# Performance work log

Hardware: AMD Instinct MI355X
Metric: run time of the kernel (lower is better)

Reference implementation:

```python
import jax, jax.numpy as jnp
import numpy as np

# RWKV6 layer dims (from init_kwargs + fla defaults)
H, DK, DV, NH = 512, 256, 512, 4          # hidden, key_dim, value_dim, heads
HK, HV = DK // NH, DV // NH               # 64, 128
RLOW, WLOW, ID = 32, 64, 1024             # proj_low_rank, decay_low_rank, ffn intermediate
EPS = 1e-5
B, T = 8, 1024


def layernorm(x, g, b):
    m = x.mean(-1, keepdims=True)
    v = ((x - m) ** 2).mean(-1, keepdims=True)
    return (x - m) * jax.lax.rsqrt(v + EPS) * g + b


def token_shift(x):  # shift sequence right by one, zero-pad first token
    return jnp.pad(x, ((0, 0), (1, 0), (0, 0)))[:, :-1]


def rwkv_forward(x, pre_g, pre_b, attn_g, attn_b, ffn_g, ffn_b,
                 xproj_mu, xproj_w1, xproj_w2, x_bias,
                 r_W, w_W1, w_W2, w_b, k_W, v_W, g_W, bonus,
                 gnorm_g, gnorm_b, o_W, fk_mu, fk_W, fv_W, fr_mu, fr_W):
    x0 = layernorm(x, pre_g, pre_b)                 # pre_norm (layer_idx == 0)
    h = layernorm(x0, attn_g, attn_b)               # attn_norm

    # ---- time-mix (RWKV6Attention) ----
    delta = token_shift(h) - h
    # low-rank data-dependent interpolation factors for r,w,k,v,g
    z = jnp.tanh(((h + delta * xproj_mu) @ xproj_w1.T).reshape(B, T, 5, RLOW))
    z = jnp.einsum('blnr,hnr->blnh', z, xproj_w2.reshape(H, 5, RLOW)) + x_bias
    zr, zw, zk, zv, zg = (z[:, :, i] for i in range(5))
    r = ((h + delta * zr) @ r_W.T).reshape(B, T, NH, HK)
    w = jnp.tanh((h + delta * zw) @ w_W1.T) @ w_W2.T + w_b   # decay LoRA
    lw = (-jnp.exp(w)).reshape(B, T, NH, HK)                 # log per-channel decay (< 0)
    k = ((h + delta * zk) @ k_W.T).reshape(B, T, NH, HK)
    v = ((h + delta * zv) @ v_W.T).reshape(B, T, NH, HV)
    g = (h + delta * zg) @ g_W.T

    # WKV6 selective-decay linear recurrence, state S: [B,NH,HK,HV]
    def step(S, inp):
        r_t, k_t, v_t, lw_t = inp
        kv = k_t[..., :, None] * v_t[..., None, :]
        o_t = jnp.einsum('bhk,bhkv->bhv', r_t, S + bonus[None, :, :, None] * kv)
        return jnp.exp(lw_t)[..., None] * S + kv, o_t

    S0 = jnp.zeros((B, NH, HK, HV), x.dtype)
    tfirst = lambda a: jnp.swapaxes(a, 0, 1)
    _, o = jax.lax.scan(step, S0, (tfirst(r), tfirst(k), tfirst(v), tfirst(lw)))
    o = jnp.swapaxes(o, 0, 1)                        # [B,T,NH,HV]

    # GroupNorm(num_heads) over value channels, then swish gate and output proj
    mu = o.mean(-1, keepdims=True)
    var = ((o - mu) ** 2).mean(-1, keepdims=True)
    o = ((o - mu) * jax.lax.rsqrt(var + EPS)).reshape(B, T, DV) * gnorm_g + gnorm_b
    a = (o * (g * jax.nn.sigmoid(g))) @ o_W.T

    res = x0 + a

    # ---- channel-mix (RWKV6FeedForward) ----
    hf = layernorm(res, ffn_g, ffn_b)
    d2 = token_shift(hf) - hf
    kk = jnp.square(jax.nn.relu((hf + d2 * fk_mu) @ fk_W.T))
    val = kk @ fv_W.T
    rec = jax.nn.sigmoid((hf + d2 * fr_mu) @ fr_W.T)
    return res + rec * val


def setup_inputs():
    key = jax.random.key(0)
    ks = iter(jax.random.split(key, 40))
    n = lambda shape, s=0.02: jax.random.normal(next(ks), shape, jnp.float32) * s
    u = lambda shape: jax.random.uniform(next(ks), shape, dtype=jnp.float32)
    return dict(
        x=jax.random.normal(next(ks), (B, T, H), jnp.float32),
        pre_g=jnp.ones(H), pre_b=jnp.zeros(H),
        attn_g=jnp.ones(H), attn_b=jnp.zeros(H),
        ffn_g=jnp.ones(H), ffn_b=jnp.zeros(H),
        xproj_mu=u((H,)), xproj_w1=n((5 * RLOW, H)), xproj_w2=n((H, 5 * RLOW)),
        x_bias=n((5, H)),
        r_W=n((DK, H)),
        w_W1=n((WLOW, H)), w_W2=n((DK, WLOW)), w_b=n((DK,), 0.5),
        k_W=n((DK, H)), v_W=n((DV, H)), g_W=n((DV, H)),
        bonus=n((NH, HK), 0.5),
        gnorm_g=jnp.ones(DV), gnorm_b=jnp.zeros(DV),
        o_W=n((H, DV)),
        fk_mu=u((H,)), fk_W=n((ID, H)),
        fv_W=n((H, ID)),
        fr_mu=u((H,)), fr_W=n((H, H)),
    )


def reference(x, pre_g, pre_b, attn_g, attn_b, ffn_g, ffn_b,
              xproj_mu, xproj_w1, xproj_w2, x_bias,
              r_W, w_W1, w_W2, w_b, k_W, v_W, g_W, bonus,
              gnorm_g, gnorm_b, o_W, fk_mu, fk_W, fv_W, fr_mu, fr_W):
    return rwkv_forward(x, pre_g, pre_b, attn_g, attn_b, ffn_g, ffn_b,
                        xproj_mu, xproj_w1, xproj_w2, x_bias,
                        r_W, w_W1, w_W2, w_b, k_W, v_W, g_W, bonus,
                        gnorm_g, gnorm_b, o_W, fk_mu, fk_W, fv_W, fr_mu, fr_W)
```

## Files before the change

kernel.cpp:

```cpp
#include <hip/hip_runtime.h>


#define DEVINL __device__ __forceinline__

constexpr int B_  = 8, T_ = 1024;
constexpr int BT_ = B_ * T_;
constexpr float EPS_ = 1e-5f;
constexpr int CH_ = 16;
constexpr int NC_ = T_ / CH_;

typedef __bf16 bf16x8 __attribute__((ext_vector_type(8)));
typedef float  f32x4  __attribute__((ext_vector_type(4)));

DEVINL unsigned short f2bs(float f) {
  union { float f; unsigned int i; } c; c.f = f;
  unsigned int x = c.i;
  return (unsigned short)((x + 0x7fffu + ((x >> 16) & 1u)) >> 16);
}
DEVINL float b2f(unsigned short u) {
  union { unsigned int i; float f; } c; c.i = ((unsigned int)u) << 16; return c.f;
}

DEVINL float block_sum256(float v, float* sb) {
  for (int o = 32; o; o >>= 1) v += __shfl_down(v, o);
  int w = threadIdx.x >> 6;
  __syncthreads();
  if ((threadIdx.x & 63) == 0) sb[w] = v;
  __syncthreads();
  return sb[0] + sb[1] + sb[2] + sb[3];
}

DEVINL void gload16(const unsigned short* gsrc, unsigned short* ldsbase) {
  __builtin_amdgcn_global_load_lds(
      (const __attribute__((address_space(1))) unsigned int*)gsrc,
      (__attribute__((address_space(3))) unsigned int*)ldsbase, 16, 0, 0);
}

struct PackSeg { const float* src; int rows, cols, dst_rows; };
struct PackArgs { PackSeg s[12]; int base[13]; };

__global__ __launch_bounds__(256) void pack_kernel(PackArgs pa, unsigned short* dst)
{
  int i = blockIdx.x * 256 + threadIdx.x;
  if (i >= pa.base[12]) return;
  int k = 0;
  while (i >= pa.base[k + 1]) k++;
  int loc = i - pa.base[k];
  PackSeg s = pa.s[k];
  int r = loc / s.cols, c = loc - r * s.cols;
  float v = (r < s.rows) ? s.src[(size_t)r * s.cols + c] : 0.f;
  dst[i] = f2bs(v);
}

__global__ __launch_bounds__(256) void ln2_kernel(
    const float* __restrict__ x,
    const float* __restrict__ pg, const float* __restrict__ pb,
    const float* __restrict__ ag, const float* __restrict__ ab,
    float* __restrict__ x0, unsigned short* __restrict__ h)
{
  __shared__ float sb[4];
  size_t base = (size_t)blockIdx.x * 512;
  int tid = threadIdx.x;
  float v0 = x[base + tid], v1 = x[base + 256 + tid];
  float m = block_sum256(v0 + v1, sb) * (1.f / 512.f);
  float d0 = v0 - m, d1 = v1 - m;
  float var = block_sum256(d0 * d0 + d1 * d1, sb) * (1.f / 512.f);
  float rs = rsqrtf(var + EPS_);
  float a0 = d0 * rs * pg[tid]       + pb[tid];
  float a1 = d1 * rs * pg[tid + 256] + pb[tid + 256];
  x0[base + tid] = a0; x0[base + 256 + tid] = a1;
  float m2 = block_sum256(a0 + a1, sb) * (1.f / 512.f);
  float e0 = a0 - m2, e1 = a1 - m2;
  float var2 = block_sum256(e0 * e0 + e1 * e1, sb) * (1.f / 512.f);
  float rs2 = rsqrtf(var2 + EPS_);
  h[base + tid]       = f2bs(e0 * rs2 * ag[tid]       + ab[tid]);
  h[base + 256 + tid] = f2bs(e1 * rs2 * ag[tid + 256] + ab[tid + 256]);
}

__global__ __launch_bounds__(256) void ln1_kernel(
    const float* __restrict__ in,
    const float* __restrict__ g, const float* __restrict__ b,
    float* __restrict__ out)
{
  __shared__ float sb[4];
  size_t base = (size_t)blockIdx.x * 512;
  int tid = threadIdx.x;
  float v0 = in[base + tid], v1 = in[base + 256 + tid];
  float m = block_sum256(v0 + v1, sb) * (1.f / 512.f);
  float d0 = v0 - m, d1 = v1 - m;
  float var = block_sum256(d0 * d0 + d1 * d1, sb) * (1.f / 512.f);
  float rs = rsqrtf(var + EPS_);
  out[base + tid]       = d0 * rs * g[tid]       + b[tid];
  out[base + 256 + tid] = d1 * rs * g[tid + 256] + b[tid + 256];
}

__global__ __launch_bounds__(256) void ymix_kernel(
    const unsigned short* __restrict__ h, const float* __restrict__ mu,
    unsigned short* __restrict__ y, unsigned short* __restrict__ dl)
{
  int t = blockIdx.x, tid = threadIdx.x, tt = t & (T_ - 1);
  size_t base = (size_t)t * 512;
  for (int c = tid; c < 512; c += 256) {
    float cur  = b2f(h[base + c]);
    float prev = tt ? b2f(h[base - 512 + c]) : 0.f;
    float d = prev - cur;
    dl[base + c] = f2bs(d);
    y[base + c] = f2bs(cur + d * mu[c]);
  }
}

__global__ __launch_bounds__(256) void ffnmix_kernel(
    const float* __restrict__ hf, const float* __restrict__ fkmu,
    const float* __restrict__ frmu,
    unsigned short* __restrict__ mfk, unsigned short* __restrict__ mfr)
{
  int t = blockIdx.x, tid = threadIdx.x, tt = t & (T_ - 1);
  size_t base = (size_t)t * 512;
  for (int c = tid; c < 512; c += 256) {
    float cur  = hf[base + c];
    float prev = tt ? hf[base - 512 + c] : 0.f;
    float d = prev - cur;
    mfk[base + c] = f2bs(cur + d * fkmu[c]);
    mfr[base + c] = f2bs(cur + d * frmu[c]);
  }
}

enum { EP_NONE_F32 = 0, EP_NONE_BF16 = 1, EP_TANH_BF16 = 2, EP_EXPEXP_F32 = 3,
       EP_RES_F32 = 4, EP_RELU2_BF16 = 5, EP_OUT2_F32 = 6, EP_XMIX_BF16 = 7 };

struct GemmDesc {
  const unsigned short* A; const unsigned short* W; void* C;
  const void* bias; const void* aux1; const void* aux2;
  int N, K, lda, ldw, ldc, epi;
};
template <int NG> struct GD { GemmDesc d[NG]; };

template <int BM, int BN, int NG>
__global__ __launch_bounds__(256) void mgemm(GD<NG> p)
{
  GemmDesc dd = p.d[blockIdx.z];
  int n0 = blockIdx.y * BN;
  if (n0 >= dd.N) return;
  int m0 = blockIdx.x * BM;
  constexpr int MFR = BM / 32, NFR = BN / 32;
  constexpr int AIS = BM / 64, WIS = BN / 64;
  constexpr int NLD = AIS + WIS;
  __shared__ unsigned short LDSbuf[2 * (BM + BN) * 32];
  unsigned short* As = LDSbuf;
  unsigned short* Ws = LDSbuf + 2 * BM * 32;
  int tid = threadIdx.x, lane = tid & 63, wid = tid >> 6;
  int wm = wid >> 1, wn = wid & 1, lrow = lane & 15, lkg = lane >> 4;
  int XL = (lrow & 3) ^ ((lrow >> 2) & 3);

  const unsigned short* aSrc[AIS]; int aOff[AIS];
#pragma unroll
  for (int i = 0; i < AIS; i++) {
    int u = i * 256 + wid * 64 + lane;
    int row = u >> 2;
    int kg = (u & 3) ^ (row & 3) ^ ((row >> 2) & 3);
    aSrc[i] = dd.A + (size_t)(m0 + row) * dd.lda + kg * 8;
    aOff[i] = (i * 256 + wid * 64) * 8;
  }
  const unsigned short* wSrc[WIS]; int wOff[WIS];
#pragma unroll
  for (int i = 0; i < WIS; i++) {
    int u = i * 256 + wid * 64 + lane;
    int row = u >> 2;
    int kg = (u & 3) ^ (row & 3) ^ ((row >> 2) & 3);
    wSrc[i] = dd.W + (size_t)(n0 + row) * dd.ldw + kg * 8;
    wOff[i] = (i * 256 + wid * 64) * 8;
  }

  f32x4 acc[MFR][NFR];
#pragma unroll
  for (int mf = 0; mf < MFR; mf++)
#pragma unroll
    for (int nf = 0; nf < NFR; nf++) acc[mf][nf] = (f32x4){0.f, 0.f, 0.f, 0.f};

#pragma unroll
  for (int i = 0; i < AIS; i++) gload16(aSrc[i], As + aOff[i]);
#pragma unroll
  for (int i = 0; i < WIS; i++) gload16(wSrc[i], Ws + wOff[i]);

  int nt = dd.K >> 5;
  for (int t = 0; t < nt; ++t) {
    int cb = t & 1;
    int pbuf = cb ^ 1;
    if (t + 1 < nt) {
      int kb2 = (t + 1) << 5;
      unsigned short* aD = As + pbuf * (BM * 32);
      unsigned short* wD = Ws + pbuf * (BN * 32);
#pragma unroll
      for (int i = 0; i < AIS; i++) gload16(aSrc[i] + kb2, aD + aOff[i]);
#pragma unroll
      for (int i = 0; i < WIS; i++) gload16(wSrc[i] + kb2, wD + wOff[i]);
      if constexpr (NLD == 4) asm volatile("s_waitcnt vmcnt(4)" ::: "memory");
      else                    asm volatile("s_waitcnt vmcnt(2)" ::: "memory");
    } else {
      asm volatile("s_waitcnt vmcnt(0)" ::: "memory");
    }
    __builtin_amdgcn_sched_barrier(0);
    __builtin_amdgcn_s_barrier();

    const unsigned short* AsB = As + cb * (BM * 32);
    const unsigned short* WsB = Ws + cb * (BN * 32);
    bf16x8 bfrag[NFR];
#pragma unroll
    for (int nf = 0; nf < NFR; nf++) {
      int row = (wn * NFR + nf) * 16 + lrow;
      bfrag[nf] = *(const bf16x8*)&WsB[(row * 4 + (lkg ^ XL)) * 8];
    }
#pragma unroll
    for (int mf = 0; mf < MFR; mf++) {
      int row = (wm * MFR + mf) * 16 + lrow;
      bf16x8 afrag = *(const bf16x8*)&AsB[(row * 4 + (lkg ^ XL)) * 8];
#pragma unroll
      for (int nf = 0; nf < NFR; nf++)
        acc[mf][nf] = __builtin_amdgcn_mfma_f32_16x16x32_bf16(
            bfrag[nf], afrag, acc[mf][nf], 0, 0, 0);
    }
    __builtin_amdgcn_sched_barrier(0);
    __builtin_amdgcn_s_barrier();
  }

  bool bf16out = (dd.epi == EP_NONE_BF16 || dd.epi == EP_TANH_BF16 ||
                  dd.epi == EP_RELU2_BF16 || dd.epi == EP_XMIX_BF16);
  if (!bf16out) {
#pragma unroll
    for (int mf = 0; mf < MFR; mf++) {
#pragma unroll
      for (int nf = 0; nf < NFR; nf++) {
        int m  = m0 + wm * (MFR * 16) + mf * 16 + lrow;
        int nb = n0 + wn * (NFR * 16) + nf * 16 + lkg * 4;
        size_t off = (size_t)m * dd.ldc + nb;
        float c0 = acc[mf][nf][0], c1 = acc[mf][nf][1];
        float c2 = acc[mf][nf][2], c3 = acc[mf][nf][3];
        switch (dd.epi) {
          case EP_NONE_F32: {
            f32x4 v = {c0, c1, c2, c3};
            *(f32x4*)((float*)dd.C + off) = v; break;
          }
          case EP_EXPEXP_F32: {
            const float* bi = (const float*)dd.bias;
            f32x4 v = {expf(-expf(c0 + bi[nb + 0])), expf(-expf(c1 + bi[nb + 1])),
                       expf(-expf(c2 + bi[nb + 2])), expf(-expf(c3 + bi[nb + 3]))};
            *(f32x4*)((float*)dd.C + off) = v; break;
          }
          case EP_RES_F32: {
            f32x4 a = *(const f32x4*)((const float*)dd.aux1 + off);
            f32x4 v = {c0 + a[0], c1 + a[1], c2 + a[2], c3 + a[3]};
            *(f32x4*)((float*)dd.C + off) = v; break;
          }
          case EP_OUT2_F32: {
            f32x4 rs = *(const f32x4*)((const float*)dd.aux1 + off);
            f32x4 fr = *(const f32x4*)((const float*)dd.aux2 + off);
            f32x4 v = {rs[0] + (1.f / (1.f + expf(-fr[0]))) * c0,
                       rs[1] + (1.f / (1.f + expf(-fr[1]))) * c1,
                       rs[2] + (1.f / (1.f + expf(-fr[2]))) * c2,
                       rs[3] + (1.f / (1.f + expf(-fr[3]))) * c3};
            *(f32x4*)((float*)dd.C + off) = v; break;
          }
        }
      }
    }
    return;
  }

  unsigned short* Cs = LDSbuf;
#pragma unroll
  for (int mf = 0; mf < MFR; mf++) {
#pragma unroll
    for (int nf = 0; nf < NFR; nf++) {
      int mloc = wm * (MFR * 16) + mf * 16 + lrow;
      int nbl  = wn * (NFR * 16) + nf * 16 + lkg * 4;
      int m = m0 + mloc, nb = n0 + nbl;
      size_t off = (size_t)m * dd.ldc + nb;
      float c0 = acc[mf][nf][0], c1 = acc[mf][nf][1];
      float c2 = acc[mf][nf][2], c3 = acc[mf][nf][3];
      uint2 u;
      switch (dd.epi) {
        case EP_NONE_BF16:
          u.x = f2bs(c0) | ((unsigned)f2bs(c1) << 16);
          u.y = f2bs(c2) | ((unsigned)f2bs(c3) << 16);
          break;
        case EP_TANH_BF16:
          u.x = f2bs(tanhf(c0)) | ((unsigned)f2bs(tanhf(c1)) << 16);
          u.y = f2bs(tanhf(c2)) | ((unsigned)f2bs(tanhf(c3)) << 16);
          break;
        case EP_RELU2_BF16: {
          c0 = fmaxf(c0, 0.f); c1 = fmaxf(c1, 0.f);
          c2 = fmaxf(c2, 0.f); c3 = fmaxf(c3, 0.f);
          u.x = f2bs(c0 * c0) | ((unsigned)f2bs(c1 * c1) << 16);
          u.y = f2bs(c2 * c2) | ((unsigned)f2bs(c3 * c3) << 16);
          break;
        }
        default: {
          const float* bi = (const float*)dd.bias;
          uint2 hv = *(const uint2*)((const unsigned short*)dd.aux1 + off);
          uint2 dv = *(const uint2*)((const unsigned short*)dd.aux2 + off);
          const unsigned short* hu = (const unsigned short*)&hv;
          const unsigned short* du = (const unsigned short*)&dv;
          float r0 = b2f(hu[0]) + b2f(du[0]) * (c0 + bi[nb + 0]);
          float r1 = b2f(hu[1]) + b2f(du[1]) * (c1 + bi[nb + 1]);
          float r2 = b2f(hu[2]) + b2f(du[2]) * (c2 + bi[nb + 2]);
          float r3 = b2f(hu[3]) + b2f(du[3]) * (c3 + bi[nb + 3]);
          u.x = f2bs(r0) | ((unsigned)f2bs(r1) << 16);
          u.y = f2bs(r2) | ((unsigned)f2bs(r3) << 16);
          break;
        }
      }
      int col4 = (nbl >> 2) ^ ((mloc & 7) << 1);
      *(uint2*)&Cs[mloc * BN + col4 * 4] = u;
    }
  }
  __syncthreads();
  constexpr int JW = BN / 8;
  constexpr int UNITS = BM * JW;
  for (int it = tid; it < UNITS; it += 256) {
    int row = it / JW, j = it - row * JW;
    int e = (row & 7) << 1;
    int4 vv = *(const int4*)&Cs[row * BN + (((2 * j) ^ e) << 2)];
    *(int4*)((unsigned short*)dd.C + (size_t)(m0 + row) * dd.ldc + n0 + j * 8) = vv;
  }
}

__global__ __launch_bounds__(256) void rbk_kernel(
    const unsigned short* __restrict__ r, const unsigned short* __restrict__ k,
    const float* __restrict__ bonus, float* __restrict__ rbk)
{
  int t = blockIdx.x, tid = threadIdx.x;
  int hh = tid >> 6, j = tid & 63;
  size_t g = (size_t)t * 256 + hh * 64 + j;
  float p = b2f(r[g]) * b2f(k[g]) * bonus[hh * 64 + j];
  for (int o = 32; o; o >>= 1) p += __shfl_down(p, o);
  if (j == 0) rbk[(size_t)t * 4 + hh] = p;
}

__global__ __launch_bounds__(128) void wkv_pass1(
    const unsigned short* __restrict__ k, const float* __restrict__ ew,
    const unsigned short* __restrict__ v, unsigned short* __restrict__ Sl,
    float* __restrict__ Dp)
{
  __shared__ float kL[CH_][64], eL[CH_][64];
  int blk = blockIdx.x;
  int c = blk & (NC_ - 1), bh = blk >> 6;
  int b = bh >> 2, hh = bh & 3;
  int tid = threadIdx.x;
  size_t tbase = (size_t)b * T_ + (size_t)c * CH_;
  for (int idx = tid; idx < CH_ * 64; idx += 128) {
    int s = idx >> 6, j = idx & 63;
    size_t g = (tbase + s) * 256 + hh * 64 + j;
    kL[s][j] = b2f(k[g]); eL[s][j] = ew[g];
  }
  __syncthreads();
  float S[64];
#pragma unroll
  for (int j = 0; j < 64; j++) S[j] = 0.f;
  for (int s = 0; s < CH_; s++) {
    float vv = b2f(v[(tbase + s) * 512 + hh * 128 + tid]);
    const float4* e4p = (const float4*)&eL[s][0];
    const float4* k4p = (const float4*)&kL[s][0];
#pragma unroll
    for (int q = 0; q < 16; q++) {
      float4 e4 = e4p[q], k4 = k4p[q];
      S[4 * q + 0] = e4.x * S[4 * q + 0] + k4.x * vv;
      S[4 * q + 1] = e4.y * S[4 * q + 1] + k4.y * vv;
      S[4 * q + 2] = e4.z * S[4 * q + 2] + k4.z * vv;
      S[4 * q + 3] = e4.w * S[4 * q + 3] + k4.w * vv;
    }
  }
  size_t sbase = (size_t)blk * 8192;
#pragma unroll
  for (int j = 0; j < 64; j++) Sl[sbase + j * 128 + tid] = f2bs(S[j]);
  if (tid < 64) {
    float d = 1.f;
    for (int s = 0; s < CH_; s++) d *= eL[s][tid];
    Dp[(size_t)blk * 64 + tid] = d;
  }
}

__global__ __launch_bounds__(256) void wkv_scan(
    const unsigned short* __restrict__ Sl, const float* __restrict__ Dp,
    unsigned short* __restrict__ Ss)
{
  int e = blockIdx.x * 256 + threadIdx.x;
  int bh = e >> 13; int kv = e & 8191; int j = kv >> 7;
  float run = 0.f;
  for (int c = 0; c < NC_; c++) {
    size_t base = (size_t)bh * NC_ + c;
    Ss[base * 8192 + kv] = f2bs(run);
    run = Dp[base * 64 + j] * run + b2f(Sl[base * 8192 + kv]);
  }
}

__global__ __launch_bounds__(128) void wkv_pass3(
    const unsigned short* __restrict__ r, const unsigned short* __restrict__ k,
    const float* __restrict__ ew, const unsigned short* __restrict__ v,
    const float* __restrict__ rbk, const unsigned short* __restrict__ Ss,
    float* __restrict__ o)
{
  __shared__ float rL[CH_][64], kL[CH_][64], eL[CH_][64], rbL[CH_];
  int blk = blockIdx.x;
  int c = blk & (NC_ - 1), bh = blk >> 6;
  int b = bh >> 2, hh = bh & 3;
  int tid = threadIdx.x;
  size_t tbase = (size_t)b * T_ + (size_t)c * CH_;
  for (int idx = tid; idx < CH_ * 64; idx += 128) {
    int s = idx >> 6, j = idx & 63;
    size_t g = (tbase + s) * 256 + hh * 64 + j;
    rL[s][j] = b2f(r[g]); kL[s][j] = b2f(k[g]); eL[s][j] = ew[g];
  }
  if (tid < CH_) rbL[tid] = rbk[(tbase + tid) * 4 + hh];
  __syncthreads();
  float S[64];
  size_t sbase = (size_t)blk * 8192;
#pragma unroll
  for (int j = 0; j < 64; j++) S[j] = b2f(Ss[sbase + j * 128 + tid]);
  for (int s = 0; s < CH_; s++) {
    float vv = b2f(v[(tbase + s) * 512 + hh * 128 + tid]);
    float oa = rbL[s] * vv;
    const float4* r4p = (const float4*)&rL[s][0];
    const float4* e4p = (const float4*)&eL[s][0];
    const float4* k4p = (const float4*)&kL[s][0];
#pragma unroll
    for (int q = 0; q < 16; q++) {
      float4 r4 = r4p[q], e4 = e4p[q], k4 = k4p[q];
      oa += r4.x * S[4 * q + 0] + r4.y * S[4 * q + 1]
          + r4.z * S[4 * q + 2] + r4.w * S[4 * q + 3];
      S[4 * q + 0] = e4.x * S[4 * q + 0] + k4.x * vv;
      S[4 * q + 1] = e4.y * S[4 * q + 1] + k4.y * vv;
      S[4 * q + 2] = e4.z * S[4 * q + 2] + k4.z * vv;
      S[4 * q + 3] = e4.w * S[4 * q + 3] + k4.w * vv;
    }
    o[(tbase + s) * 512 + hh * 128 + tid] = oa;
  }
}

__global__ __launch_bounds__(256) void gn_gate_kernel(
    const float* __restrict__ o, const unsigned short* __restrict__ g,
    const float* __restrict__ gg, const float* __restrict__ gb,
    unsigned short* __restrict__ obf)
{
  __shared__ float ov[512], ps[64], qs[64], mh[4], vh[4];
  int t = blockIdx.x, tid = threadIdx.x;
  size_t base = (size_t)t * 512;
  ov[tid] = o[base + tid]; ov[tid + 256] = o[base + 256 + tid];
  __syncthreads();
  if (tid < 64) {
    int hh = tid >> 4, sg = tid & 15;
    const float* p = &ov[hh * 128 + sg * 8];
    float s = 0.f, q = 0.f;
    for (int i = 0; i < 8; i++) { s += p[i]; q += p[i] * p[i]; }
    ps[tid] = s; qs[tid] = q;
  }
  __syncthreads();
  if (tid < 4) {
    float s = 0.f, q = 0.f;
    for (int i = 0; i < 16; i++) { s += ps[tid * 16 + i]; q += qs[tid * 16 + i]; }
    float m = s * (1.f / 128.f);
    mh[tid] = m; vh[tid] = q * (1.f / 128.f) - m * m;
  }
  __syncthreads();
  for (int c = tid; c < 512; c += 256) {
    int hh = c >> 7;
    float nrm = (ov[c] - mh[hh]) * rsqrtf(vh[hh] + EPS_);
    float gv = b2f(g[base + c]);
    float sw = gv * (1.f / (1.f + expf(-gv)));
    obf[base + c] = f2bs((nrm * gg[c] + gb[c]) * sw);
  }
}

extern "C" void kernel_launch(void* const* d_in, const int* in_sizes, int n_in,
                              void* d_out, int out_size, void* d_ws, size_t ws_size,
                              hipStream_t stream) {
  (void)in_sizes; (void)n_in; (void)out_size; (void)ws_size;
  const float* x        = (const float*)d_in[0];
  const float* pre_g    = (const float*)d_in[1];
  const float* pre_b    = (const float*)d_in[2];
  const float* attn_g   = (const float*)d_in[3];
  const float* attn_b   = (const float*)d_in[4];
  const float* ffn_g    = (const float*)d_in[5];
  const float* ffn_b    = (const float*)d_in[6];
  const float* xproj_mu = (const float*)d_in[7];
  const float* xproj_w1 = (const float*)d_in[8];
  const float* xproj_w2 = (const float*)d_in[9];
  const float* x_bias   = (const float*)d_in[10];
  const float* r_W      = (const float*)d_in[11];
  const float* w_W1     = (const float*)d_in[12];
  const float* w_W2     = (const float*)d_in[13];
  const float* w_b      = (const float*)d_in[14];
  const float* k_W      = (const float*)d_in[15];
  const float* v_W      = (const float*)d_in[16];
  const float* g_W      = (const float*)d_in[17];
  const float* bonus    = (const float*)d_in[18];
  const float* gnorm_g  = (const float*)d_in[19];
  const float* gnorm_b  = (const float*)d_in[20];
  const float* o_W      = (const float*)d_in[21];
  const float* fk_mu    = (const float*)d_in[22];
  const float* fk_W     = (const float*)d_in[23];
  const float* fv_W     = (const float*)d_in[24];
  const float* fr_mu    = (const float*)d_in[25];
  const float* fr_W     = (const float*)d_in[26];

  const size_t BTH = (size_t)BT_ * 512;
  size_t cur = 0;
  auto alloc = [&](size_t bytes) { void* p = (char*)d_ws + cur; cur += (bytes + 255) & ~(size_t)255; return p; };
  float*          x0    = (float*)alloc(BTH * 4);
  unsigned short* hbufb = (unsigned short*)alloc(BTH * 2);
  unsigned short* m5b   = (unsigned short*)alloc(5 * BTH * 2);
  unsigned short* rbuf  = (unsigned short*)alloc((size_t)BT_ * 256 * 4);
  unsigned short* kbuf  = (unsigned short*)alloc((size_t)BT_ * 256 * 4);
  float*          ebuf  = (float*)alloc((size_t)BT_ * 256 * 4);
  unsigned short* vbuf  = (unsigned short*)alloc(BTH * 4);
  unsigned short* gbuf  = (unsigned short*)alloc(BTH * 4);
  unsigned short* wtmpb = (unsigned short*)alloc((size_t)BT_ * 128 * 2);
  float*          rbk   = (float*)alloc((size_t)BT_ * 4 * 4);
  unsigned short* Sl    = (unsigned short*)alloc((size_t)2048 * 8192 * 2);
  unsigned short* Ss    = (unsigned short*)alloc((size_t)2048 * 8192 * 2);
  float*          Dp    = (float*)alloc((size_t)2048 * 64 * 4);
  float*          res   = (float*)alloc(BTH * 4);
  unsigned short* wpack = (unsigned short*)alloc((size_t)2621440 * 2);
  unsigned short* ybufb = rbuf;
  unsigned short* dlb   = vbuf;
  unsigned short* z5b   = gbuf;
  float*          obuf  = (float*)m5b;
  unsigned short* obf16 = (unsigned short*)ebuf;
  float*          hf    = x0;
  unsigned short* mfk   = rbuf;
  unsigned short* mfr   = kbuf;
  unsigned short* kkb   = Sl;
  float*          frtmp = (float*)vbuf;

  PackArgs pa;
  int off = 0, seg = 0;
  auto addseg = [&](const float* src, int rows, int cols, int dst_rows) {
    pa.s[seg] = {src, rows, cols, dst_rows};
    pa.base[seg] = off; off += dst_rows * cols; seg++;
  };
  addseg(xproj_w1, 160, 512, 192);   int o_w1p = pa.base[0];
  addseg(w_W1,      64, 512, 128);   int o_wW1 = pa.base[1];
  addseg(r_W,      256, 512, 256);   int o_rW  = pa.base[2];
  addseg(k_W,      256, 512, 256);   int o_kW  = pa.base[3];
  addseg(v_W,      512, 512, 512);   int o_vW  = pa.base[4];
  addseg(g_W,      512, 512, 512);   int o_gW  = pa.base[5];
  addseg(o_W,      512, 512, 512);   int o_oW  = pa.base[6];
  addseg(fk_W,    1024, 512, 1024);  int o_fkW = pa.base[7];
  addseg(fv_W,     512, 1024, 512);  int o_fvW = pa.base[8];
  addseg(fr_W,     512, 512, 512);   int o_frW = pa.base[9];
  addseg(w_W2,     256, 64, 256);    int o_wW2 = pa.base[10];
  addseg(xproj_w2, 512, 160, 512);   int o_xw2 = pa.base[11];
  pa.base[12] = off;

  pack_kernel<<<(off + 255) / 256, 256, 0, stream>>>(pa, wpack);
  ln2_kernel<<<BT_, 256, 0, stream>>>(x, pre_g, pre_b, attn_g, attn_b, x0, hbufb);
  ymix_kernel<<<BT_, 256, 0, stream>>>(hbufb, xproj_mu, ybufb, dlb);

  auto solo = [&](const unsigned short* A, const unsigned short* W, void* C,
                  const void* bias, const void* a1, const void* a2,
                  int N, int K, int lda, int ldw, int ldc, int epi) {
    GD<1> g; g.d[0] = {A, W, C, bias, a1, a2, N, K, lda, ldw, ldc, epi};
    mgemm<64, 64, 1><<<dim3(128, (N + 63) / 64, 1), 256, 0, stream>>>(g);
  };

  solo(ybufb, wpack + o_w1p, z5b, nullptr, nullptr, nullptr,
       192, 512, 512, 512, 192, EP_TANH_BF16);

  {
    GD<5> g;
    for (int n = 0; n < 5; n++)
      g.d[n] = {z5b + n * 32, wpack + o_xw2 + n * 32, m5b + (size_t)n * BTH,
                x_bias + n * 512, hbufb, dlb, 512, 32, 192, 160, 512, EP_XMIX_BF16};
    mgemm<128, 128, 5><<<dim3(64, 4, 5), 256, 0, stream>>>(g);
  }

  {
    GD<5> g;
    g.d[0] = {m5b + 0 * BTH, wpack + o_rW, rbuf, nullptr, nullptr, nullptr, 256, 512, 512, 512, 256, EP_NONE_BF16};
    g.d[1] = {m5b + 1 * BTH, wpack + o_wW1, wtmpb, nullptr, nullptr, nullptr, 128, 512, 512, 512, 128, EP_TANH_BF16};
    g.d[2] = {m5b + 2 * BTH, wpack + o_kW, kbuf, nullptr, nullptr, nullptr, 256, 512, 512, 512, 256, EP_NONE_BF16};
    g.d[3] = {m5b + 3 * BTH, wpack + o_vW, vbuf, nullptr, nullptr, nullptr, 512, 512, 512, 512, 512, EP_NONE_BF16};
    g.d[4] = {m5b + 4 * BTH, wpack + o_gW, gbuf, nullptr, nullptr, nullptr, 512, 512, 512, 512, 512, EP_NONE_BF16};
    mgemm<128, 128, 5><<<dim3(64, 4, 5), 256, 0, stream>>>(g);
  }

  solo(wtmpb, wpack + o_wW2, ebuf, w_b, nullptr, nullptr,
       256, 64, 128, 64, 256, EP_EXPEXP_F32);

  rbk_kernel<<<BT_, 256, 0, stream>>>(rbuf, kbuf, bonus, rbk);
  wkv_pass1<<<2048, 128, 0, stream>>>(kbuf, ebuf, vbuf, Sl, Dp);
  wkv_scan<<<1024, 256, 0, stream>>>(Sl, Dp, Ss);
  wkv_pass3<<<2048, 128, 0, stream>>>(rbuf, kbuf, ebuf, vbuf, rbk, Ss, obuf);

  gn_gate_kernel<<<BT_, 256, 0, stream>>>(obuf, gbuf, gnorm_g, gnorm_b, obf16);

  solo(obf16, wpack + o_oW, res, nullptr, x0, nullptr,
       512, 512, 512, 512, 512, EP_RES_F32);

  ln1_kernel<<<BT_, 256, 0, stream>>>(res, ffn_g, ffn_b, hf);
  ffnmix_kernel<<<BT_, 256, 0, stream>>>(hf, fk_mu, fr_mu, mfk, mfr);

  {
    GD<2> g;
    g.d[0] = {mfk, wpack + o_fkW, kkb, nullptr, nullptr, nullptr, 1024, 512, 512, 512, 1024, EP_RELU2_BF16};
    g.d[1] = {mfr, wpack + o_frW, frtmp, nullptr, nullptr, nullptr, 512, 512, 512, 512, 512, EP_NONE_F32};
    mgemm<128, 128, 2><<<dim3(64, 8, 2), 256, 0, stream>>>(g);
  }

  solo(kkb, wpack + o_fvW, (float*)d_out, nullptr, res, frtmp,
       512, 1024, 1024, 1024, 512, EP_OUT2_F32);
}
```

Baseline: 310.9 us.

## Deepen GEMM global-to-LDS prefetch from double to triple buffering

The multi-GEMM kernel now keeps three LDS stages and prefetches two K-tiles ahead instead of one, with the vmcnt waits adjusted so the current tile's loads are complete before use. The goal is to hide more global memory latency behind the MFMA work. The cost is 1.5x the LDS footprint, which can lower occupancy, plus an extra barrier before the LDS-staged bf16 epilogue. These GEMMs have small K (mostly 512 or 1024), so the deeper pipeline has few iterations over which to pay off.

```diff
diff --git a/kernel.cpp b/kernel.cpp
--- a/kernel.cpp
+++ b/kernel.cpp
@@ -145,9 +145,9 @@
   constexpr int MFR = BM / 32, NFR = BN / 32;
   constexpr int AIS = BM / 64, WIS = BN / 64;
   constexpr int NLD = AIS + WIS;
-  __shared__ unsigned short LDSbuf[2 * (BM + BN) * 32];
-  unsigned short* As = LDSbuf;
-  unsigned short* Ws = LDSbuf + 2 * BM * 32;
+  __shared__ unsigned short LDSbuf[3 * (BM + BN) * 32];
+  unsigned short* AsBase = LDSbuf;
+  unsigned short* WsBase = LDSbuf + 3 * BM * 32;
   int tid = threadIdx.x, lane = tid & 63, wid = tid >> 6;
   int wm = wid >> 1, wn = wid & 1, lrow = lane & 15, lkg = lane >> 4;
   int XL = (lrow & 3) ^ ((lrow >> 2) & 3);
@@ -177,23 +177,32 @@
 #pragma unroll
     for (int nf = 0; nf < NFR; nf++) acc[mf][nf] = (f32x4){0.f, 0.f, 0.f, 0.f};
 
-#pragma unroll
-  for (int i = 0; i < AIS; i++) gload16(aSrc[i], As + aOff[i]);
-#pragma unroll
-  for (int i = 0; i < WIS; i++) gload16(wSrc[i], Ws + wOff[i]);
-
   int nt = dd.K >> 5;
+#pragma unroll
+  for (int i = 0; i < AIS; i++) gload16(aSrc[i], AsBase + aOff[i]);
+#pragma unroll
+  for (int i = 0; i < WIS; i++) gload16(wSrc[i], WsBase + wOff[i]);
+  if (nt > 1) {
+#pragma unroll
+    for (int i = 0; i < AIS; i++) gload16(aSrc[i] + 32, AsBase + BM * 32 + aOff[i]);
+#pragma unroll
+    for (int i = 0; i < WIS; i++) gload16(wSrc[i] + 32, WsBase + BN * 32 + wOff[i]);
+  }
+
+  int cur = 0, pf = 2;
   for (int t = 0; t < nt; ++t) {
-    int cb = t & 1;
-    int pbuf = cb ^ 1;
-    if (t + 1 < nt) {
-      int kb2 = (t + 1) << 5;
-      unsigned short* aD = As + pbuf * (BM * 32);
-      unsigned short* wD = Ws + pbuf * (BN * 32);
+    if (t + 2 < nt) {
+      int kb2 = (t + 2) << 5;
+      unsigned short* aD = AsBase + pf * (BM * 32);
+      unsigned short* wD = WsBase + pf * (BN * 32);
 #pragma unroll
       for (int i = 0; i < AIS; i++) gload16(aSrc[i] + kb2, aD + aOff[i]);
 #pragma unroll
       for (int i = 0; i < WIS; i++) gload16(wSrc[i] + kb2, wD + wOff[i]);
+      pf = (pf == 2) ? 0 : pf + 1;
+      if constexpr (NLD == 4) asm volatile("s_waitcnt vmcnt(8)" ::: "memory");
+      else                    asm volatile("s_waitcnt vmcnt(4)" ::: "memory");
+    } else if (t + 1 < nt) {
       if constexpr (NLD == 4) asm volatile("s_waitcnt vmcnt(4)" ::: "memory");
       else                    asm volatile("s_waitcnt vmcnt(2)" ::: "memory");
     } else {
@@ -202,8 +211,8 @@
     __builtin_amdgcn_sched_barrier(0);
     __builtin_amdgcn_s_barrier();
 
-    const unsigned short* AsB = As + cb * (BM * 32);
-    const unsigned short* WsB = Ws + cb * (BN * 32);
+    const unsigned short* AsB = AsBase + cur * (BM * 32);
+    const unsigned short* WsB = WsBase + cur * (BN * 32);
     bf16x8 bfrag[NFR];
 #pragma unroll
     for (int nf = 0; nf < NFR; nf++) {
@@ -221,6 +230,7 @@
     }
     __builtin_amdgcn_sched_barrier(0);
     __builtin_amdgcn_s_barrier();
+    cur = (cur == 2) ? 0 : cur + 1;
   }
 
   bool bf16out = (dd.epi == EP_NONE_BF16 || dd.epi == EP_TANH_BF16 ||
@@ -266,6 +276,7 @@
     return;
   }
 
+  __syncthreads();
   unsigned short* Cs = LDSbuf;
 #pragma unroll
   for (int mf = 0; mf < MFR; mf++) {
```

Result: no change. 310.5 us (-0.1%).

## Replace 4-wave GEMM blocks with single-wave 64x64 tiles without barriers

Applied to the files above, without the earlier changes.

All GEMM launches now use a one-wavefront kernel that computes a 64x64 tile per block (4x4 MFMA fragments per wave), instead of 256-thread blocks with 64x64 or 128x128 tiles split over four waves. Because each wave loads and consumes its own LDS tiles, the s_barrier and __syncthreads calls are removed and only vmcnt waits remain. This trades the reuse of larger tiles and shared loads for many more small blocks and no inter-wave synchronisation, with more global traffic per FLOP for the grouped GEMMs.

```diff
diff --git a/kernel.cpp b/kernel.cpp
--- a/kernel.cpp
+++ b/kernel.cpp
@@ -135,103 +135,85 @@
 };
 template <int NG> struct GD { GemmDesc d[NG]; };
 
-template <int BM, int BN, int NG>
-__global__ __launch_bounds__(256) void mgemm(GD<NG> p)
+template <int NG>
+__global__ __launch_bounds__(64) void mgemm64(GD<NG> p)
 {
   GemmDesc dd = p.d[blockIdx.z];
-  int n0 = blockIdx.y * BN;
+  int n0 = blockIdx.y * 64;
   if (n0 >= dd.N) return;
-  int m0 = blockIdx.x * BM;
-  constexpr int MFR = BM / 32, NFR = BN / 32;
-  constexpr int AIS = BM / 64, WIS = BN / 64;
-  constexpr int NLD = AIS + WIS;
-  __shared__ unsigned short LDSbuf[2 * (BM + BN) * 32];
-  unsigned short* As = LDSbuf;
-  unsigned short* Ws = LDSbuf + 2 * BM * 32;
-  int tid = threadIdx.x, lane = tid & 63, wid = tid >> 6;
-  int wm = wid >> 1, wn = wid & 1, lrow = lane & 15, lkg = lane >> 4;
+  int m0 = blockIdx.x * 64;
+  __shared__ unsigned short LDSbuf[4 * 2048];
+  unsigned short* AsBase = LDSbuf;
+  unsigned short* WsBase = LDSbuf + 2 * 2048;
+  int lane = threadIdx.x;
+  int lrow = lane & 15, lkg = lane >> 4;
   int XL = (lrow & 3) ^ ((lrow >> 2) & 3);
 
-  const unsigned short* aSrc[AIS]; int aOff[AIS];
-#pragma unroll
-  for (int i = 0; i < AIS; i++) {
-    int u = i * 256 + wid * 64 + lane;
+  const unsigned short* aSrc[4]; const unsigned short* wSrc[4]; int uOff[4];
+#pragma unroll
+  for (int i = 0; i < 4; i++) {
+    int u = i * 64 + lane;
     int row = u >> 2;
     int kg = (u & 3) ^ (row & 3) ^ ((row >> 2) & 3);
     aSrc[i] = dd.A + (size_t)(m0 + row) * dd.lda + kg * 8;
-    aOff[i] = (i * 256 + wid * 64) * 8;
-  }
-  const unsigned short* wSrc[WIS]; int wOff[WIS];
-#pragma unroll
-  for (int i = 0; i < WIS; i++) {
-    int u = i * 256 + wid * 64 + lane;
-    int row = u >> 2;
-    int kg = (u & 3) ^ (row & 3) ^ ((row >> 2) & 3);
     wSrc[i] = dd.W + (size_t)(n0 + row) * dd.ldw + kg * 8;
-    wOff[i] = (i * 256 + wid * 64) * 8;
-  }
-
-  f32x4 acc[MFR][NFR];
-#pragma unroll
-  for (int mf = 0; mf < MFR; mf++)
-#pragma unroll
-    for (int nf = 0; nf < NFR; nf++) acc[mf][nf] = (f32x4){0.f, 0.f, 0.f, 0.f};
-
-#pragma unroll
-  for (int i = 0; i < AIS; i++) gload16(aSrc[i], As + aOff[i]);
-#pragma unroll
-  for (int i = 0; i < WIS; i++) gload16(wSrc[i], Ws + wOff[i]);
+    uOff[i] = i * 64 * 8;
+  }
+
+  f32x4 acc[4][4];
+#pragma unroll
+  for (int mf = 0; mf < 4; mf++)
+#pragma unroll
+    for (int nf = 0; nf < 4; nf++) acc[mf][nf] = (f32x4){0.f, 0.f, 0.f, 0.f};
+
+#pragma unroll
+  for (int i = 0; i < 4; i++) gload16(aSrc[i], AsBase + uOff[i]);
+#pragma unroll
+  for (int i = 0; i < 4; i++) gload16(wSrc[i], WsBase + uOff[i]);
 
   int nt = dd.K >> 5;
   for (int t = 0; t < nt; ++t) {
     int cb = t & 1;
-    int pbuf = cb ^ 1;
     if (t + 1 < nt) {
       int kb2 = (t + 1) << 5;
-      unsigned short* aD = As + pbuf * (BM * 32);
-      unsigned short* wD = Ws + pbuf * (BN * 32);
-#pragma unroll
-      for (int i = 0; i < AIS; i++) gload16(aSrc[i] + kb2, aD + aOff[i]);
-#pragma unroll
-      for (int i = 0; i < WIS; i++) gload16(wSrc[i] + kb2, wD + wOff[i]);
-      if constexpr (NLD == 4) asm volatile("s_waitcnt vmcnt(4)" ::: "memory");
-      else                    asm volatile("s_waitcnt vmcnt(2)" ::: "memory");
+      unsigned short* aD = AsBase + (cb ^ 1) * 2048;
+      unsigned short* wD = WsBase + (cb ^ 1) * 2048;
+#pragma unroll
+      for (int i = 0; i < 4; i++) gload16(aSrc[i] + kb2, aD + uOff[i]);
+#pragma unroll
+      for (int i = 0; i < 4; i++) gload16(wSrc[i] + kb2, wD + uOff[i]);
+      asm volatile("s_waitcnt vmcnt(8)" ::: "memory");
     } else {
       asm volatile("s_waitcnt vmcnt(0)" ::: "memory");
     }
     __builtin_amdgcn_sched_barrier(0);
-    __builtin_amdgcn_s_barrier();
-
-    const unsigned short* AsB = As + cb * (BM * 32);
-    const unsigned short* WsB = Ws + cb * (BN * 32);
-    bf16x8 bfrag[NFR];
-#pragma unroll
-    for (int nf = 0; nf < NFR; nf++) {
-      int row = (wn * NFR + nf) * 16 + lrow;
-      bfrag[nf] = *(const bf16x8*)&WsB[(row * 4 + (lkg ^ XL)) * 8];
-    }
-#pragma unroll
-    for (int mf = 0; mf < MFR; mf++) {
-      int row = (wm * MFR + mf) * 16 + lrow;
-      bf16x8 afrag = *(const bf16x8*)&AsB[(row * 4 + (lkg ^ XL)) * 8];
-#pragma unroll
-      for (int nf = 0; nf < NFR; nf++)
+
+    const unsigned short* AsB = AsBase + cb * 2048;
+    const unsigned short* WsB = WsBase + cb * 2048;
+    bf16x8 bfrag[4];
+#pragma unroll
+    for (int nf = 0; nf < 4; nf++)
+      bfrag[nf] = *(const bf16x8*)&WsB[((nf * 16 + lrow) * 4 + (lkg ^ XL)) * 8];
+#pragma unroll
+    for (int mf = 0; mf < 4; mf++) {
+      bf16x8 afrag = *(const bf16x8*)&AsB[((mf * 16 + lrow) * 4 + (lkg ^ XL)) * 8];
+#pragma unroll
+      for (int nf = 0; nf < 4; nf++)
         acc[mf][nf] = __builtin_amdgcn_mfma_f32_16x16x32_bf16(
             bfrag[nf], afrag, acc[mf][nf], 0, 0, 0);
     }
     __builtin_amdgcn_sched_barrier(0);
-    __builtin_amdgcn_s_barrier();
   }
 
   bool bf16out = (dd.epi == EP_NONE_BF16 || dd.epi == EP_TANH_BF16 ||
                   dd.epi == EP_RELU2_BF16 || dd.epi == EP_XMIX_BF16);
   if (!bf16out) {
 #pragma unroll
-    for (int mf = 0; mf < MFR; mf++) {
-#pragma unroll
-      for (int nf = 0; nf < NFR; nf++) {
-        int m  = m0 + wm * (MFR * 16) + mf * 16 + lrow;
-        int nb = n0 + wn * (NFR * 16) + nf * 16 + lkg * 4;
+    for (int mf = 0; mf < 4; mf++) {
+#pragma unroll
+      for (int nf = 0; nf < 4; nf++) {
+        int m  = m0 + mf * 16 + lrow;
+        int nb = n0 + nf * 16 + lkg * 4;
         size_t off = (size_t)m * dd.ldc + nb;
         float c0 = acc[mf][nf][0], c1 = acc[mf][nf][1];
         float c2 = acc[mf][nf][2], c3 = acc[mf][nf][3];
@@ -268,11 +250,11 @@
 
   unsigned short* Cs = LDSbuf;
 #pragma unroll
-  for (int mf = 0; mf < MFR; mf++) {
-#pragma unroll
-    for (int nf = 0; nf < NFR; nf++) {
-      int mloc = wm * (MFR * 16) + mf * 16 + lrow;
-      int nbl  = wn * (NFR * 16) + nf * 16 + lkg * 4;
+  for (int mf = 0; mf < 4; mf++) {
+#pragma unroll
+    for (int nf = 0; nf < 4; nf++) {
+      int mloc = mf * 16 + lrow;
+      int nbl  = nf * 16 + lkg * 4;
       int m = m0 + mloc, nb = n0 + nbl;
       size_t off = (size_t)m * dd.ldc + nb;
       float c0 = acc[mf][nf][0], c1 = acc[mf][nf][1];
@@ -310,16 +292,13 @@
         }
       }
       int col4 = (nbl >> 2) ^ ((mloc & 7) << 1);
-      *(uint2*)&Cs[mloc * BN + col4 * 4] = u;
+      *(uint2*)&Cs[mloc * 64 + col4 * 4] = u;
     }
   }
-  __syncthreads();
-  constexpr int JW = BN / 8;
-  constexpr int UNITS = BM * JW;
-  for (int it = tid; it < UNITS; it += 256) {
-    int row = it / JW, j = it - row * JW;
+  for (int it = lane; it < 512; it += 64) {
+    int row = it >> 3, j = it & 7;
     int e = (row & 7) << 1;
-    int4 vv = *(const int4*)&Cs[row * BN + (((2 * j) ^ e) << 2)];
+    int4 vv = *(const int4*)&Cs[row * 64 + (((2 * j) ^ e) << 2)];
     *(int4*)((unsigned short*)dd.C + (size_t)(m0 + row) * dd.ldc + n0 + j * 8) = vv;
   }
 }
@@ -559,7 +538,7 @@
                   const void* bias, const void* a1, const void* a2,
                   int N, int K, int lda, int ldw, int ldc, int epi) {
     GD<1> g; g.d[0] = {A, W, C, bias, a1, a2, N, K, lda, ldw, ldc, epi};
-    mgemm<64, 64, 1><<<dim3(128, (N + 63) / 64, 1), 256, 0, stream>>>(g);
+    mgemm64<1><<<dim3(128, (N + 63) / 64, 1), 64, 0, stream>>>(g);
   };
 
   solo(ybufb, wpack + o_w1p, z5b, nullptr, nullptr, nullptr,
@@ -570,7 +549,7 @@
     for (int n = 0; n < 5; n++)
       g.d[n] = {z5b + n * 32, wpack + o_xw2 + n * 32, m5b + (size_t)n * BTH,
                 x_bias + n * 512, hbufb, dlb, 512, 32, 192, 160, 512, EP_XMIX_BF16};
-    mgemm<128, 128, 5><<<dim3(64, 4, 5), 256, 0, stream>>>(g);
+    mgemm64<5><<<dim3(128, 8, 5), 64, 0, stream>>>(g);
   }
 
   {
@@ -580,7 +559,7 @@
     g.d[2] = {m5b + 2 * BTH, wpack + o_kW, kbuf, nullptr, nullptr, nullptr, 256, 512, 512, 512, 256, EP_NONE_BF16};
     g.d[3] = {m5b + 3 * BTH, wpack + o_vW, vbuf, nullptr, nullptr, nullptr, 512, 512, 512, 512, 512, EP_NONE_BF16};
     g.d[4] = {m5b + 4 * BTH, wpack + o_gW, gbuf, nullptr, nullptr, nullptr, 512, 512, 512, 512, 512, EP_NONE_BF16};
-    mgemm<128, 128, 5><<<dim3(64, 4, 5), 256, 0, stream>>>(g);
+    mgemm64<5><<<dim3(128, 8, 5), 64, 0, stream>>>(g);
   }
 
   solo(wtmpb, wpack + o_wW2, ebuf, w_b, nullptr, nullptr,
@@ -603,7 +582,7 @@
     GD<2> g;
     g.d[0] = {mfk, wpack + o_fkW, kkb, nullptr, nullptr, nullptr, 1024, 512, 512, 512, 1024, EP_RELU2_BF16};
     g.d[1] = {mfr, wpack + o_frW, frtmp, nullptr, nullptr, nullptr, 512, 512, 512, 512, 512, EP_NONE_F32};
-    mgemm<128, 128, 2><<<dim3(64, 8, 2), 256, 0, stream>>>(g);
+    mgemm64<2><<<dim3(128, 16, 2), 64, 0, stream>>>(g);
   }
 
   solo(kkb, wpack + o_fvW, (float*)d_out, nullptr, res, frtmp,
```

Measured after the change: 419.7 us. 1.35x slower.
